# Optimization experiments

Hardware: AMD Instinct MI355X
Metric: run time of the kernel (lower is better)

The kernel has to match this reference:

```python
import math
import jax, jax.numpy as jnp
import numpy as np

HEAD_DIM = 128
N_HEADS = 64    # n_local_heads
N_KV = 8        # n_local_kv_heads
N_REP = 8       # GQA group size


def setup_inputs() -> dict:
    key = jax.random.key(0)
    ks = jax.random.split(key, 6)
    bsz, seqlen, d = 32, 1, 8192
    start_pos = 4095
    T = start_pos + seqlen  # 4096 total KV length
    x = jax.random.normal(ks[0], (bsz, seqlen, d), jnp.float32)
    wqkv_w = jax.random.normal(ks[1], (8192, 10240), jnp.float32) * 0.02  # used as x @ W
    wo_w = jax.random.normal(ks[2], (8192, 8192), jnp.float32) * 0.02    # torch Linear weight (out,in)
    theta = jax.random.uniform(ks[3], (seqlen, HEAD_DIM // 2), jnp.float32) * (2.0 * np.pi)
    freqs_cos = jnp.cos(theta)
    freqs_sin = jnp.sin(theta)
    cache_k = jax.random.normal(ks[4], (bsz, T, N_KV, HEAD_DIM), jnp.float32)
    cache_v = jax.random.normal(ks[5], (bsz, T, N_KV, HEAD_DIM), jnp.float32)
    mask = jnp.zeros((1, 1, 1, T), jnp.float32)
    return {"x": x, "cache_k": cache_k, "cache_v": cache_v, "wqkv_w": wqkv_w,
            "wo_w": wo_w, "freqs_cos": freqs_cos, "freqs_sin": freqs_sin,
            "mask": mask, "start_pos": start_pos}


def _rope(t, cos, sin):
    # t: [b, s, h, d]; cos/sin: [s, d//2]. Complex mult on interleaved (re, im) pairs.
    tr = t.reshape(*t.shape[:-1], -1, 2)
    c = cos[None, :, None, :]
    s = sin[None, :, None, :]
    re = tr[..., 0] * c - tr[..., 1] * s
    im = tr[..., 0] * s + tr[..., 1] * c
    return jnp.stack([re, im], axis=-1).reshape(t.shape)


def reference(x, cache_k, cache_v, wqkv_w, wo_w, freqs_cos, freqs_sin, mask, start_pos):
    bsz, seqlen, _ = x.shape
    blk_q = N_REP * HEAD_DIM  # 1024
    blk = blk_q + HEAD_DIM + HEAD_DIM  # 1280: interleaved q|k|v block
    # fused qkv projection, then split interleaved blocks
    xqkv = jnp.einsum('bsd,dn->bsn', x, wqkv_w).reshape(bsz, seqlen, -1, blk)
    xq = xqkv[..., :blk_q].reshape(bsz, seqlen, N_HEADS, HEAD_DIM)
    xk = xqkv[..., blk_q:blk_q + HEAD_DIM].reshape(bsz, seqlen, N_KV, HEAD_DIM)
    xv = xqkv[..., blk_q + HEAD_DIM:].reshape(bsz, seqlen, N_KV, HEAD_DIM)
    # rotary embedding on q and k
    xq = _rope(xq, freqs_cos, freqs_sin)
    xk = _rope(xk, freqs_cos, freqs_sin)
    # KV-cache write
    cache_k = jax.lax.dynamic_update_slice(cache_k, xk, (0, start_pos, 0, 0))
    cache_v = jax.lax.dynamic_update_slice(cache_v, xv, (0, start_pos, 0, 0))
    T = start_pos + seqlen
    keys = cache_k[:, :T]     # [b, T, kv, d]
    values = cache_v[:, :T]
    # GQA: group q-heads by kv-head instead of materializing repeat_kv (same math)
    q = xq.transpose(0, 2, 1, 3).reshape(bsz, N_KV, N_REP, seqlen, HEAD_DIM)
    scores = jnp.einsum('bkrsd,btkd->bkrst', q, keys) / math.sqrt(HEAD_DIM)
    scores = scores + mask  # mask [1,1,1,T] broadcasts over (r, s, t)
    probs = jax.nn.softmax(scores, axis=-1)
    out = jnp.einsum('bkrst,btkd->bkrsd', probs, values)
    out = out.reshape(bsz, N_HEADS, seqlen, HEAD_DIM).transpose(0, 2, 1, 3).reshape(bsz, seqlen, -1)
    return out @ wo_w.T
```

## Files before the change

### kernel.cpp

```cpp
#include <hip/hip_runtime.h>
#include <hip/hip_bf16.h>
#include <math.h>

typedef float  f32x4 __attribute__((ext_vector_type(4)));
typedef short  s16x8 __attribute__((ext_vector_type(8)));
typedef unsigned int u32;

#define B_   32
#define D_   8192
#define NQ   10240
#define T_   4096
#define NKV  8
#define HD   128
#define BLKW 1280
#define KSPLIT 16
#define KC   512

__device__ inline short f2bf(float f) {
  union { float f; unsigned u; } v; v.f = f;
  unsigned r = (v.u + 0x7FFFu + ((v.u >> 16) & 1u)) >> 16;
  return (short)r;
}

__device__ inline s16x8 pack8(float4 a, float4 b) {
  s16x8 r;
  r[0]=f2bf(a.x); r[1]=f2bf(a.y); r[2]=f2bf(a.z); r[3]=f2bf(a.w);
  r[4]=f2bf(b.x); r[5]=f2bf(b.y); r[6]=f2bf(b.z); r[7]=f2bf(b.w);
  return r;
}

__global__ __launch_bounds__(256) void k_qkv(const float* __restrict__ x,
                                             const float* __restrict__ W,
                                             float* __restrict__ p1) {
  __shared__ float wtile[2][32 * 128];
  int tid  = threadIdx.x;
  int lane = tid & 63, wv = tid >> 6;
  int l15  = lane & 15, lg = lane >> 4;
  int nblk = blockIdx.x * 128;
  int n0   = nblk + wv * 32;
  int k0   = blockIdx.y * KC;

  f32x4 acc00 = (f32x4)0.f, acc01 = (f32x4)0.f;
  f32x4 acc10 = (f32x4)0.f, acc11 = (f32x4)0.f;

  const float* xr0 = x + (size_t)l15 * D_ + k0 + lg * 8;
  const float* xr1 = x + (size_t)(16 + l15) * D_ + k0 + lg * 8;

  #define STAGE(buf, ks)                                                        \
    {                                                                           \
      const float* src = W + (size_t)(k0 + (ks)) * NQ + nblk;                   \
      _Pragma("unroll")                                                         \
      for (int i = 0; i < 4; ++i) {                                             \
        int p = i * 256 + tid;                                                  \
        const float* gp = src + (size_t)(p >> 5) * NQ + (p & 31) * 4;           \
        __builtin_amdgcn_global_load_lds(                                       \
            (const __attribute__((address_space(1))) u32*)gp,                   \
            (__attribute__((address_space(3))) u32*)&wtile[buf][p * 4],         \
            16, 0, 0);                                                          \
      }                                                                         \
    }

  STAGE(0, 0);
  __syncthreads();

  int buf = 0;
  for (int ks = 0; ks < KC; ks += 32) {
    if (ks + 32 < KC) STAGE(buf ^ 1, ks + 32);

    float4 a0a = *(const float4*)(xr0 + ks);
    float4 a0b = *(const float4*)(xr0 + ks + 4);
    float4 a1a = *(const float4*)(xr1 + ks);
    float4 a1b = *(const float4*)(xr1 + ks + 4);
    s16x8 af0 = pack8(a0a, a0b);
    s16x8 af1 = pack8(a1a, a1b);

    const float* wt = &wtile[buf][wv * 32 + l15];
    s16x8 bf0, bf1;
    #pragma unroll
    for (int j = 0; j < 8; ++j) {
      float w0 = wt[(lg * 8 + j) * 128];
      float w1 = wt[(lg * 8 + j) * 128 + 16];
      bf0[j] = f2bf(w0);
      bf1[j] = f2bf(w1);
    }

    acc00 = __builtin_amdgcn_mfma_f32_16x16x32_bf16(af0, bf0, acc00, 0, 0, 0);
    acc01 = __builtin_amdgcn_mfma_f32_16x16x32_bf16(af0, bf1, acc01, 0, 0, 0);
    acc10 = __builtin_amdgcn_mfma_f32_16x16x32_bf16(af1, bf0, acc10, 0, 0, 0);
    acc11 = __builtin_amdgcn_mfma_f32_16x16x32_bf16(af1, bf1, acc11, 0, 0, 0);

    __syncthreads();
    buf ^= 1;
  }
  #undef STAGE

  size_t base = (size_t)(blockIdx.y * 32) * NQ;
  #pragma unroll
  for (int r = 0; r < 4; ++r) {
    p1[base + (size_t)(lg * 4 + r) * NQ + n0 + l15]           = acc00[r];
    p1[base + (size_t)(lg * 4 + r) * NQ + n0 + 16 + l15]      = acc01[r];
    p1[base + (size_t)(16 + lg * 4 + r) * NQ + n0 + l15]      = acc10[r];
    p1[base + (size_t)(16 + lg * 4 + r) * NQ + n0 + 16 + l15] = acc11[r];
  }
}

__global__ void k_reduce_rope(const float* __restrict__ p1,
                              const float* __restrict__ fcos, const float* __restrict__ fsin,
                              float* __restrict__ qs, float* __restrict__ knew,
                              float* __restrict__ vnew) {
  int b = blockIdx.y;
  int j = (blockIdx.x * 256 + threadIdx.x) * 2;
  float v0 = 0.f, v1 = 0.f;
  #pragma unroll
  for (int c = 0; c < KSPLIT; ++c) {
    const float2 p = *(const float2*)(p1 + (size_t)(c * 32 + b) * NQ + j);
    v0 += p.x; v1 += p.y;
  }
  int g = j / BLKW;
  int r = j - g * BLKW;
  if (r < 1024) {
    int h = r >> 7, d = r & 127, dp = d >> 1;
    float c = fcos[dp], s = fsin[dp];
    const float sc = 0.08838834764831845f;
    float* q = qs + ((size_t)(b * NKV + g) * 8 + h) * HD + d;
    q[0] = (v0 * c - v1 * s) * sc;
    q[1] = (v0 * s + v1 * c) * sc;
  } else if (r < 1152) {
    int d = r - 1024, dp = d >> 1;
    float c = fcos[dp], s = fsin[dp];
    float* kp = knew + (size_t)(b * NKV + g) * HD + d;
    kp[0] = v0 * c - v1 * s;
    kp[1] = v0 * s + v1 * c;
  } else {
    int d = r - 1152;
    float* vp = vnew + (size_t)(b * NKV + g) * HD + d;
    vp[0] = v0; vp[1] = v1;
  }
}

__global__ __launch_bounds__(256) void k_attn(const float* __restrict__ cK,
                                              const float* __restrict__ cV,
                                              const float* __restrict__ qs,
                                              const float* __restrict__ knew,
                                              const float* __restrict__ vnew,
                                              float* __restrict__ pml,
                                              float* __restrict__ pacc) {
  __shared__ __align__(16) short Plds[4][2][16][32];
  int bid  = blockIdx.x;
  int pair = bid >> 2, tc = bid & 3;
  int b = pair >> 3, kv = pair & 7;
  int tid = threadIdx.x;
  int w = tid >> 6, lane = tid & 63;
  int l15 = lane & 15, lg = lane >> 4;

  for (int idx = lane; idx < 512; idx += 64) {
    int buf = idx >> 8, rem = idx & 255;
    Plds[w][buf][8 + (rem >> 5)][rem & 31] = 0;
  }

  s16x8 aq[4];
  const float* qrow = qs + ((size_t)(b * NKV + kv) * 8 + l15) * HD;
  #pragma unroll
  for (int dt = 0; dt < 4; ++dt) {
    if (l15 < 8) {
      float4 fa = *(const float4*)(qrow + dt * 32 + lg * 8);
      float4 fb = *(const float4*)(qrow + dt * 32 + lg * 8 + 4);
      aq[dt] = pack8(fa, fb);
    } else {
      s16x8 z = {0,0,0,0,0,0,0,0};
      aq[dt] = z;
    }
  }

  float m[4], lsum[4];
  #pragma unroll
  for (int r = 0; r < 4; ++r) { m[r] = -INFINITY; lsum[r] = 0.f; }
  f32x4 acc[8];
  #pragma unroll
  for (int dt = 0; dt < 8; ++dt) acc[dt] = (f32x4)0.f;

  const size_t bkv_off = (size_t)b * T_ * NKV * HD + (size_t)kv * HD;
  const float* knp = knew + (size_t)(b * NKV + kv) * HD;
  const float* vnp = vnew + (size_t)(b * NKV + kv) * HD;

  for (int tile = 0; tile < 8; ++tile) {
    int t0 = tc * 1024 + (w * 8 + tile) * 32;
    int pb = tile & 1;

    f32x4 s0 = (f32x4)0.f, s1 = (f32x4)0.f;
    {
      int trow = t0 + l15;
      const float* krow = (trow == 4095) ? knp : (cK + bkv_off + (size_t)trow * (NKV * HD));
      #pragma unroll
      for (int dt = 0; dt < 4; ++dt) {
        float4 fa = *(const float4*)(krow + dt * 32 + lg * 8);
        float4 fb = *(const float4*)(krow + dt * 32 + lg * 8 + 4);
        s16x8 bk = pack8(fa, fb);
        s0 = __builtin_amdgcn_mfma_f32_16x16x32_bf16(aq[dt], bk, s0, 0, 0, 0);
      }
    }
    {
      int trow = t0 + 16 + l15;
      const float* krow = (trow == 4095) ? knp : (cK + bkv_off + (size_t)trow * (NKV * HD));
      #pragma unroll
      for (int dt = 0; dt < 4; ++dt) {
        float4 fa = *(const float4*)(krow + dt * 32 + lg * 8);
        float4 fb = *(const float4*)(krow + dt * 32 + lg * 8 + 4);
        s16x8 bk = pack8(fa, fb);
        s1 = __builtin_amdgcn_mfma_f32_16x16x32_bf16(aq[dt], bk, s1, 0, 0, 0);
      }
    }

    float p0[4], p1v[4], scale[4];
    #pragma unroll
    for (int r = 0; r < 4; ++r) {
      float tm = fmaxf(s0[r], s1[r]);
      #pragma unroll
      for (int off = 1; off < 16; off <<= 1) tm = fmaxf(tm, __shfl_xor(tm, off));
      float mn = fmaxf(m[r], tm);
      scale[r] = __expf(m[r] - mn);
      p0[r]  = __expf(s0[r] - mn);
      p1v[r] = __expf(s1[r] - mn);
      float rsum = p0[r] + p1v[r];
      #pragma unroll
      for (int off = 1; off < 16; off <<= 1) rsum += __shfl_xor(rsum, off);
      lsum[r] = lsum[r] * scale[r] + rsum;
      m[r] = mn;
    }
    #pragma unroll
    for (int dt = 0; dt < 8; ++dt) {
      #pragma unroll
      for (int r = 0; r < 4; ++r) acc[dt][r] *= scale[r];
    }

    if (lg < 2) {
      #pragma unroll
      for (int r = 0; r < 4; ++r) {
        int h = lg * 4 + r;
        Plds[w][pb][h][l15]      = f2bf(p0[r]);
        Plds[w][pb][h][16 + l15] = f2bf(p1v[r]);
      }
    }
    asm volatile("s_waitcnt lgkmcnt(0)" ::: "memory");
    s16x8 ap = *(const s16x8*)&Plds[w][pb][l15][lg * 8];

    const float* vrow[8];
    #pragma unroll
    for (int jj = 0; jj < 8; ++jj) {
      int tr = t0 + lg * 8 + jj;
      vrow[jj] = (tr == 4095) ? vnp : (cV + bkv_off + (size_t)tr * (NKV * HD));
    }
    #pragma unroll
    for (int dt = 0; dt < 8; ++dt) {
      s16x8 bv;
      #pragma unroll
      for (int jj = 0; jj < 8; ++jj) bv[jj] = f2bf(vrow[jj][dt * 16 + l15]);
      acc[dt] = __builtin_amdgcn_mfma_f32_16x16x32_bf16(ap, bv, acc[dt], 0, 0, 0);
    }
  }

  int widx = bid * 4 + w;
  if (lg < 2) {
    #pragma unroll
    for (int r = 0; r < 4; ++r) {
      int h = lg * 4 + r;
      if (l15 == 0) {
        pml[widx * 16 + h]     = m[r];
        pml[widx * 16 + 8 + h] = lsum[r];
      }
      #pragma unroll
      for (int dt = 0; dt < 8; ++dt)
        pacc[(size_t)widx * 1024 + h * 128 + dt * 16 + l15] = acc[dt][r];
    }
  }
}

__global__ void k_attn_combine(const float* __restrict__ pml,
                               const float* __restrict__ pacc,
                               float* __restrict__ o) {
  int pair = blockIdx.x;
  int tid = threadIdx.x;
  #pragma unroll
  for (int cc = 0; cc < 4; ++cc) {
    int cell = cc * 256 + tid;
    int h = cell >> 7;
    float mstar = -INFINITY;
    #pragma unroll
    for (int w2 = 0; w2 < 16; ++w2)
      mstar = fmaxf(mstar, pml[(pair * 16 + w2) * 16 + h]);
    float L = 0.f, val = 0.f;
    #pragma unroll
    for (int w2 = 0; w2 < 16; ++w2) {
      float mw = pml[(pair * 16 + w2) * 16 + h];
      float lw = pml[(pair * 16 + w2) * 16 + 8 + h];
      float f = __expf(mw - mstar);
      L += lw * f;
      val += f * pacc[(size_t)(pair * 16 + w2) * 1024 + cell];
    }
    o[(size_t)pair * 1024 + cell] = val / L;
  }
}

__global__ __launch_bounds__(256) void k_oproj(const float* __restrict__ o,
                                               const float* __restrict__ wo,
                                               float* __restrict__ p2) {
  int tid = threadIdx.x;
  int w = tid >> 6, lane = tid & 63, l15 = lane & 15, lg = lane >> 4;
  int i0 = blockIdx.x * 64 + w * 16;
  int jc = blockIdx.y * 1024;
  f32x4 acc0 = (f32x4)0.f, acc1 = (f32x4)0.f;
  const float* orow0 = o + (size_t)l15 * D_;
  const float* orow1 = o + (size_t)(16 + l15) * D_;
  const float* wrow  = wo + (size_t)(i0 + l15) * D_;
  for (int j = jc; j < jc + 1024; j += 32) {
    int off = j + lg * 8;
    float4 a0 = *(const float4*)(orow0 + off), a0b = *(const float4*)(orow0 + off + 4);
    float4 a1 = *(const float4*)(orow1 + off), a1b = *(const float4*)(orow1 + off + 4);
    float4 b0 = *(const float4*)(wrow + off),  b0b = *(const float4*)(wrow + off + 4);
    s16x8 fa0 = pack8(a0, a0b);
    s16x8 fa1 = pack8(a1, a1b);
    s16x8 fb  = pack8(b0, b0b);
    acc0 = __builtin_amdgcn_mfma_f32_16x16x32_bf16(fa0, fb, acc0, 0, 0, 0);
    acc1 = __builtin_amdgcn_mfma_f32_16x16x32_bf16(fa1, fb, acc1, 0, 0, 0);
  }
  size_t base = (size_t)blockIdx.y * (B_ * D_);
  #pragma unroll
  for (int r = 0; r < 4; ++r) {
    p2[base + (size_t)(lg * 4 + r) * D_ + i0 + l15]      = acc0[r];
    p2[base + (size_t)(16 + lg * 4 + r) * D_ + i0 + l15] = acc1[r];
  }
}

__global__ void k_final(const float* __restrict__ p2, float* __restrict__ out) {
  int g = blockIdx.x * 256 + threadIdx.x;
  float s = 0.f;
  #pragma unroll
  for (int c = 0; c < 8; ++c) s += p2[(size_t)c * (B_ * D_) + g];
  out[g] = s;
}

extern "C" void kernel_launch(void* const* d_in, const int* in_sizes, int n_in,
                              void* d_out, int out_size, void* d_ws, size_t ws_size,
                              hipStream_t stream) {
  const float* x    = (const float*)d_in[0];
  const float* cK   = (const float*)d_in[1];
  const float* cV   = (const float*)d_in[2];
  const float* wqkv = (const float*)d_in[3];
  const float* wo   = (const float*)d_in[4];
  const float* fcos = (const float*)d_in[5];
  const float* fsin = (const float*)d_in[6];

  float* W = (float*)d_ws;
  float* qs     = W + 262144;
  float* knew   = W + 524288;
  float* vnew   = W + 557056;
  float* o      = W + 589824;
  float* shared = W + 851968;
  float* p1   = shared;
  float* pml  = shared;
  float* pacc = shared + 65536;
  float* p2   = shared;
  float* outF = (float*)d_out;

  k_qkv<<<dim3(80, KSPLIT), 256, 0, stream>>>(x, wqkv, p1);
  k_reduce_rope<<<dim3(20, 32), 256, 0, stream>>>(p1, fcos, fsin, qs, knew, vnew);
  k_attn<<<1024, 256, 0, stream>>>(cK, cV, qs, knew, vnew, pml, pacc);
  k_attn_combine<<<256, 256, 0, stream>>>(pml, pacc, o);
  k_oproj<<<dim3(128, 8), 256, 0, stream>>>(o, wo, p2);
  k_final<<<1024, 256, 0, stream>>>(p2, outF);
}
```

Measured before the change: 445.6 us.

## Use packed bf16 conversion instruction and prefetch x operands in QKV GEMM

Replaces the software round-to-nearest-even float-to-bf16 conversion with the hardware v_cvt_pk_bf16_f32 instruction, which converts two floats per instruction. It is applied in the QKV GEMM and in the attention PV path. It also software-pipelines the x activation loads one iteration ahead in the QKV loop and removes an explicit lgkmcnt wait before reading P from LDS. The changes target the ALU cost of conversion and load latency. Dropping the wait relies on the compiler inserting the required LDS dependency waits itself.

```diff
diff --git a/kernel.cpp b/kernel.cpp
--- a/kernel.cpp
+++ b/kernel.cpp
@@ -22,11 +22,19 @@
   return (short)r;
 }
 
+__device__ inline u32 cvtpk(float lo, float hi) {
+  u32 r;
+  asm("v_cvt_pk_bf16_f32 %0, %1, %2" : "=v"(r) : "v"(lo), "v"(hi));
+  return r;
+}
+
 __device__ inline s16x8 pack8(float4 a, float4 b) {
-  s16x8 r;
-  r[0]=f2bf(a.x); r[1]=f2bf(a.y); r[2]=f2bf(a.z); r[3]=f2bf(a.w);
-  r[4]=f2bf(b.x); r[5]=f2bf(b.y); r[6]=f2bf(b.z); r[7]=f2bf(b.w);
-  return r;
+  union { u32 u[4]; s16x8 s; } r;
+  r.u[0] = cvtpk(a.x, a.y);
+  r.u[1] = cvtpk(a.z, a.w);
+  r.u[2] = cvtpk(b.x, b.y);
+  r.u[3] = cvtpk(b.z, b.w);
+  return r.s;
 }
 
 __global__ __launch_bounds__(256) void k_qkv(const float* __restrict__ x,
@@ -61,33 +69,44 @@
     }
 
   STAGE(0, 0);
+
+  float4 nx0a = *(const float4*)(xr0);
+  float4 nx0b = *(const float4*)(xr0 + 4);
+  float4 nx1a = *(const float4*)(xr1);
+  float4 nx1b = *(const float4*)(xr1 + 4);
+
   __syncthreads();
 
   int buf = 0;
   for (int ks = 0; ks < KC; ks += 32) {
     if (ks + 32 < KC) STAGE(buf ^ 1, ks + 32);
 
-    float4 a0a = *(const float4*)(xr0 + ks);
-    float4 a0b = *(const float4*)(xr0 + ks + 4);
-    float4 a1a = *(const float4*)(xr1 + ks);
-    float4 a1b = *(const float4*)(xr1 + ks + 4);
-    s16x8 af0 = pack8(a0a, a0b);
-    s16x8 af1 = pack8(a1a, a1b);
+    float4 c0a = nx0a, c0b = nx0b, c1a = nx1a, c1b = nx1b;
+    if (ks + 32 < KC) {
+      nx0a = *(const float4*)(xr0 + ks + 32);
+      nx0b = *(const float4*)(xr0 + ks + 36);
+      nx1a = *(const float4*)(xr1 + ks + 32);
+      nx1b = *(const float4*)(xr1 + ks + 36);
+    }
+    s16x8 af0 = pack8(c0a, c0b);
+    s16x8 af1 = pack8(c1a, c1b);
 
     const float* wt = &wtile[buf][wv * 32 + l15];
-    s16x8 bf0, bf1;
-    #pragma unroll
-    for (int j = 0; j < 8; ++j) {
-      float w0 = wt[(lg * 8 + j) * 128];
-      float w1 = wt[(lg * 8 + j) * 128 + 16];
-      bf0[j] = f2bf(w0);
-      bf1[j] = f2bf(w1);
-    }
-
-    acc00 = __builtin_amdgcn_mfma_f32_16x16x32_bf16(af0, bf0, acc00, 0, 0, 0);
-    acc01 = __builtin_amdgcn_mfma_f32_16x16x32_bf16(af0, bf1, acc01, 0, 0, 0);
-    acc10 = __builtin_amdgcn_mfma_f32_16x16x32_bf16(af1, bf0, acc10, 0, 0, 0);
-    acc11 = __builtin_amdgcn_mfma_f32_16x16x32_bf16(af1, bf1, acc11, 0, 0, 0);
+    union { u32 u[4]; s16x8 s; } bf0, bf1;
+    #pragma unroll
+    for (int j = 0; j < 4; ++j) {
+      float w0a = wt[(lg * 8 + 2 * j) * 128];
+      float w0b = wt[(lg * 8 + 2 * j + 1) * 128];
+      float w1a = wt[(lg * 8 + 2 * j) * 128 + 16];
+      float w1b = wt[(lg * 8 + 2 * j + 1) * 128 + 16];
+      bf0.u[j] = cvtpk(w0a, w0b);
+      bf1.u[j] = cvtpk(w1a, w1b);
+    }
+
+    acc00 = __builtin_amdgcn_mfma_f32_16x16x32_bf16(af0, bf0.s, acc00, 0, 0, 0);
+    acc01 = __builtin_amdgcn_mfma_f32_16x16x32_bf16(af0, bf1.s, acc01, 0, 0, 0);
+    acc10 = __builtin_amdgcn_mfma_f32_16x16x32_bf16(af1, bf0.s, acc10, 0, 0, 0);
+    acc11 = __builtin_amdgcn_mfma_f32_16x16x32_bf16(af1, bf1.s, acc11, 0, 0, 0);
 
     __syncthreads();
     buf ^= 1;
@@ -241,7 +260,6 @@
         Plds[w][pb][h][16 + l15] = f2bf(p1v[r]);
       }
     }
-    asm volatile("s_waitcnt lgkmcnt(0)" ::: "memory");
     s16x8 ap = *(const s16x8*)&Plds[w][pb][l15][lg * 8];
 
     const float* vrow[8];
@@ -252,10 +270,13 @@
     }
     #pragma unroll
     for (int dt = 0; dt < 8; ++dt) {
-      s16x8 bv;
-      #pragma unroll
-      for (int jj = 0; jj < 8; ++jj) bv[jj] = f2bf(vrow[jj][dt * 16 + l15]);
-      acc[dt] = __builtin_amdgcn_mfma_f32_16x16x32_bf16(ap, bv, acc[dt], 0, 0, 0);
+      float vv[8];
+      #pragma unroll
+      for (int jj = 0; jj < 8; ++jj) vv[jj] = vrow[jj][dt * 16 + l15];
+      union { u32 u[4]; s16x8 s; } bv;
+      #pragma unroll
+      for (int jj = 0; jj < 4; ++jj) bv.u[jj] = cvtpk(vv[2 * jj], vv[2 * jj + 1]);
+      acc[dt] = __builtin_amdgcn_mfma_f32_16x16x32_bf16(ap, bv.s, acc[dt], 0, 0, 0);
     }
   }
 
```

New measurement: 507.6 us. +13.9%, slower.

## Deepen QKV GEMM weight pipeline to four LDS stages with register-prefetched activations

Applied to the files above, without the earlier changes.

Replaces the double-buffered LDS staging in the QKV projection kernel with a four-slot ring. Three weight tiles are kept in flight, and activation rows are prefetched two steps ahead into registers. The per-iteration __syncthreads pair is replaced by hand-counted s_waitcnt vmcnt values plus a single s_barrier, to hide more global-memory latency on the bandwidth-bound weight stream. The cost is double the LDS use, which may reduce occupancy. Correctness also depends on the hardcoded vmcnt counts matching the exact number of outstanding loads.

```diff
diff --git a/kernel.cpp b/kernel.cpp
--- a/kernel.cpp
+++ b/kernel.cpp
@@ -32,7 +32,7 @@
 __global__ __launch_bounds__(256) void k_qkv(const float* __restrict__ x,
                                              const float* __restrict__ W,
                                              float* __restrict__ p1) {
-  __shared__ float wtile[2][32 * 128];
+  __shared__ float wtile[4][32 * 128];
   int tid  = threadIdx.x;
   int lane = tid & 63, wv = tid >> 6;
   int l15  = lane & 15, lg = lane >> 4;
@@ -46,51 +46,62 @@
   const float* xr0 = x + (size_t)l15 * D_ + k0 + lg * 8;
   const float* xr1 = x + (size_t)(16 + l15) * D_ + k0 + lg * 8;
 
-  #define STAGE(buf, ks)                                                        \
+  #define STAGE(j)                                                              \
     {                                                                           \
-      const float* src = W + (size_t)(k0 + (ks)) * NQ + nblk;                   \
+      const float* src = W + (size_t)(k0 + (j) * 32) * NQ + nblk;               \
       _Pragma("unroll")                                                         \
       for (int i = 0; i < 4; ++i) {                                             \
         int p = i * 256 + tid;                                                  \
         const float* gp = src + (size_t)(p >> 5) * NQ + (p & 31) * 4;           \
         __builtin_amdgcn_global_load_lds(                                       \
             (const __attribute__((address_space(1))) u32*)gp,                   \
-            (__attribute__((address_space(3))) u32*)&wtile[buf][p * 4],         \
+            (__attribute__((address_space(3))) u32*)&wtile[(j) & 3][p * 4],     \
             16, 0, 0);                                                          \
       }                                                                         \
     }
 
-  STAGE(0, 0);
-  __syncthreads();
-
-  int buf = 0;
-  for (int ks = 0; ks < KC; ks += 32) {
-    if (ks + 32 < KC) STAGE(buf ^ 1, ks + 32);
-
-    float4 a0a = *(const float4*)(xr0 + ks);
-    float4 a0b = *(const float4*)(xr0 + ks + 4);
-    float4 a1a = *(const float4*)(xr1 + ks);
-    float4 a1b = *(const float4*)(xr1 + ks + 4);
-    s16x8 af0 = pack8(a0a, a0b);
-    s16x8 af1 = pack8(a1a, a1b);
-
-    const float* wt = &wtile[buf][wv * 32 + l15];
+  float4 c0a = *(const float4*)(xr0);
+  float4 c0b = *(const float4*)(xr0 + 4);
+  float4 c1a = *(const float4*)(xr1);
+  float4 c1b = *(const float4*)(xr1 + 4);
+  float4 n0a = *(const float4*)(xr0 + 32);
+  float4 n0b = *(const float4*)(xr0 + 36);
+  float4 n1a = *(const float4*)(xr1 + 32);
+  float4 n1b = *(const float4*)(xr1 + 36);
+  STAGE(0); STAGE(1); STAGE(2);
+
+  for (int k = 0; k < 16; ++k) {
+    if (k == 0 || k == 14)
+      asm volatile("s_waitcnt vmcnt(8)" ::: "memory");
+    else if (k == 15)
+      asm volatile("s_waitcnt vmcnt(0)" ::: "memory");
+    else
+      asm volatile("s_waitcnt vmcnt(12)" ::: "memory");
+    __builtin_amdgcn_s_barrier();
+
+    s16x8 af0 = pack8(c0a, c0b);
+    s16x8 af1 = pack8(c1a, c1b);
+    c0a = n0a; c0b = n0b; c1a = n1a; c1b = n1b;
+    if (k + 2 < 16) {
+      n0a = *(const float4*)(xr0 + (k + 2) * 32);
+      n0b = *(const float4*)(xr0 + (k + 2) * 32 + 4);
+      n1a = *(const float4*)(xr1 + (k + 2) * 32);
+      n1b = *(const float4*)(xr1 + (k + 2) * 32 + 4);
+    }
+    if (k + 3 < 16) STAGE(k + 3);
+
+    const float* wt = &wtile[k & 3][wv * 32 + l15];
     s16x8 bf0, bf1;
     #pragma unroll
     for (int j = 0; j < 8; ++j) {
-      float w0 = wt[(lg * 8 + j) * 128];
-      float w1 = wt[(lg * 8 + j) * 128 + 16];
-      bf0[j] = f2bf(w0);
-      bf1[j] = f2bf(w1);
+      bf0[j] = f2bf(wt[(lg * 8 + j) * 128]);
+      bf1[j] = f2bf(wt[(lg * 8 + j) * 128 + 16]);
     }
 
     acc00 = __builtin_amdgcn_mfma_f32_16x16x32_bf16(af0, bf0, acc00, 0, 0, 0);
     acc01 = __builtin_amdgcn_mfma_f32_16x16x32_bf16(af0, bf1, acc01, 0, 0, 0);
     acc10 = __builtin_amdgcn_mfma_f32_16x16x32_bf16(af1, bf0, acc10, 0, 0, 0);
     acc11 = __builtin_amdgcn_mfma_f32_16x16x32_bf16(af1, bf1, acc11, 0, 0, 0);
-
-    __syncthreads();
-    buf ^= 1;
   }
   #undef STAGE
 
```

After: 443.2 us. No clear change (-0.6%).
